# Kernel tuning notes

Measured on AMD Instinct MI355X. Metric: run time of the kernel, lower is better.

The kernel has to match this reference:

```python
import jax, jax.numpy as jnp
import numpy as np

MX_D, MN_D, CENTERS, WIDTH, SLOPE = 10.0, 0.0, 16, 1.0, 0.01
T_STEPS = 3


def _lrelu(x):
    return jax.nn.leaky_relu(x, SLOPE)


def _gauss(d):
    # d: [B,E,1] distances -> [B,E,CENTERS] gaussian radial basis
    mu = jnp.linspace(MN_D, MX_D, CENTERS, dtype=d.dtype)
    return jnp.exp(-jnp.square((d - mu[None, None, :]) / WIDTH))


def _equiv_message(v, idx2, n_recv, W1, W2, b, aw, ab):
    # v: [B,E,F] = concat(sender feats, receiver feats, bond feats).
    # Outer-product expand over receiver-cell axis (einsum with one-hot),
    # permutation-equivariant linear (local term + cell-sum term), LeakyReLU,
    # gather receiver cell, sigmoid attention gate, scatter_add to receivers.
    B, E, _ = v.shape
    O = W1.shape[1]
    oh = jax.nn.one_hot(idx2, n_recv, dtype=v.dtype)                 # [E,N]
    y_loc = jnp.einsum('bef,fo->beo', v, W1)                          # per-cell term
    y_sum = jnp.einsum('bef,fo->beo', v, W2) + b                      # cell-sum term (sum_n v*oh = v)
    y = _lrelu(y_loc[..., None] * oh[None, :, None, :] + y_sum[..., None])  # [B,E,O,N]
    gidx = jnp.broadcast_to(idx2[None, :, None, None], (B, E, O, 1))
    lat = jnp.take_along_axis(y, gidx, axis=3)[..., 0]                # [B,E,O]
    lat = jax.nn.sigmoid(lat @ aw + ab[None, None, :]) * lat          # attention gating
    return jnp.zeros((B, n_recv, O), v.dtype).at[:, idx2].add(lat)    # scatter_add over receivers


def _forward(sites, bonds, sites_p, bonds_sp, bonds_ps,
             se_W, se_b, sep_W, sep_b, ee_W, ee_b, eep_W, eep_b,
             eq_W1_ss, eq_W2_ss, eq_b_ss, att_w_ss, att_b_ss,
             eq_W1_ps, eq_W2_ps, eq_b_ps, att_w_ps, att_b_ps,
             eq_W1_sp, eq_W2_sp, eq_b_sp, att_w_sp, att_b_sp,
             nu_W1, nu_b1, nu_W2, nu_b2, nup_W1, nup_b1, nup_W2, nup_b2,
             p1_W, p1_b, p2a_W, p2a_b, p2b_W, p2b_b, p3_W, p3_b,
             idx1, idx2, idx1_sp, idx2_sp, idx1_ps, idx2_ps):
    s = _lrelu(sites @ se_W + se_b)          # [B,N,D] site embedding
    sp = _lrelu(sites_p @ sep_W + sep_b)     # [B,Np,D] pore embedding
    be = _lrelu(_gauss(bonds) @ ee_W + ee_b)
    bsp = _lrelu(_gauss(bonds_sp) @ eep_W + eep_b)
    bps = _lrelu(_gauss(bonds_ps) @ eep_W + eep_b)
    N, Np = s.shape[1], sp.shape[1]
    for t in range(T_STEPS):  # fixed number of message-passing layers
        v_ss = jnp.concatenate([s[:, idx1], s[:, idx2], be], -1)
        m = _equiv_message(v_ss, idx2, N, eq_W1_ss[t], eq_W2_ss[t], eq_b_ss[t], att_w_ss[t], att_b_ss[t])
        v_ps = jnp.concatenate([sp[:, idx1_ps], s[:, idx2_ps], bps], -1)
        m_ps = _equiv_message(v_ps, idx2_ps, N, eq_W1_ps[t], eq_W2_ps[t], eq_b_ps[t], att_w_ps[t], att_b_ps[t])
        v_sp = jnp.concatenate([s[:, idx1_sp], sp[:, idx2_sp], bsp], -1)
        m_sp = _equiv_message(v_sp, idx2_sp, Np, eq_W1_sp[t], eq_W2_sp[t], eq_b_sp[t], att_w_sp[t], att_b_sp[t])
        h = jnp.concatenate([s, m, m_ps], -1)
        h = _lrelu(_lrelu(h @ nu_W1[t] + nu_b1[t]) @ nu_W2[t] + nu_b2[t])
        s = s + h                              # residual node update (sites)
        hp = jnp.concatenate([sp, m_sp], -1)
        hp = _lrelu(_lrelu(hp @ nup_W1[t] + nup_b1[t]) @ nup_W2[t] + nup_b2[t])
        sp = sp + hp                           # residual node update (pores)
    x = _lrelu(s @ p1_W + p1_b).sum(1)        # sum pool over sites
    x = _lrelu(x @ p2a_W + p2a_b)
    x = _lrelu(x @ p2b_W + p2b_b)
    return x @ p3_W + p3_b                    # [B, out_size]


def setup_inputs():
    key = jax.random.key(0)
    ks = iter(jax.random.split(key, 80))
    B, N, Np, E, Esp = 4, 128, 16, 1280, 1024
    D, C, O, M, T = 32, CENTERS, 32, 64, T_STEPS
    Fin = 2 * D + 16  # sender + receiver + edge embedding

    def nrm(shape, fan):
        return jax.random.normal(next(ks), shape, jnp.float32) / np.float32(np.sqrt(fan))

    inp = {}
    inp['sites'] = jax.random.uniform(next(ks), (B, N, 1), jnp.float32)
    inp['bonds'] = jax.random.uniform(next(ks), (B, E, 1), jnp.float32) * MX_D
    inp['sites_p'] = jax.random.uniform(next(ks), (B, Np, 2), jnp.float32)
    inp['bonds_sp'] = jax.random.uniform(next(ks), (B, Esp, 1), jnp.float32) * MX_D
    inp['bonds_ps'] = jax.random.uniform(next(ks), (B, Esp, 1), jnp.float32) * MX_D
    inp['idx1'] = jax.random.randint(next(ks), (E,), 0, N, jnp.int32)
    inp['idx2'] = jax.random.randint(next(ks), (E,), 0, N, jnp.int32)
    inp['idx1_sp'] = jax.random.randint(next(ks), (Esp,), 0, N, jnp.int32)
    inp['idx2_sp'] = jax.random.randint(next(ks), (Esp,), 0, Np, jnp.int32)
    inp['idx1_ps'] = jax.random.randint(next(ks), (Esp,), 0, Np, jnp.int32)
    inp['idx2_ps'] = jax.random.randint(next(ks), (Esp,), 0, N, jnp.int32)
    # embeddings
    inp['se_W'] = nrm((1, D), 1); inp['se_b'] = nrm((D,), D)
    inp['sep_W'] = nrm((2, D), 2); inp['sep_b'] = nrm((D,), D)
    inp['ee_W'] = nrm((C, 16), C); inp['ee_b'] = nrm((16,), 16)
    inp['eep_W'] = nrm((C, 16), C); inp['eep_b'] = nrm((16,), 16)
    # equivariant message layers (stacked over T steps)
    for suf in ('ss', 'ps', 'sp'):
        inp['eq_W1_' + suf] = nrm((T, Fin, O), Fin)
        inp['eq_W2_' + suf] = nrm((T, Fin, O), Fin)
        inp['eq_b_' + suf] = nrm((T, O), O)
        inp['att_w_' + suf] = nrm((T, O, 1), O)
        inp['att_b_' + suf] = nrm((T, 1), 1)
    # node updates: sites take 2 message streams, pores take 1
    inp['nu_W1'] = nrm((T, D + 2 * O, D), D + 2 * O); inp['nu_b1'] = nrm((T, D), D)
    inp['nu_W2'] = nrm((T, D, D), D); inp['nu_b2'] = nrm((T, D), D)
    inp['nup_W1'] = nrm((T, D + O, D), D + O); inp['nup_b1'] = nrm((T, D), D)
    inp['nup_W2'] = nrm((T, D, D), D); inp['nup_b2'] = nrm((T, D), D)
    # prediction head
    inp['p1_W'] = nrm((D, M), D); inp['p1_b'] = nrm((M,), M)
    inp['p2a_W'] = nrm((M, M), M); inp['p2a_b'] = nrm((M,), M)
    inp['p2b_W'] = nrm((M, M), M); inp['p2b_b'] = nrm((M,), M)
    inp['p3_W'] = nrm((M, 1), M); inp['p3_b'] = nrm((1,), 1)
    return inp


def reference(sites, bonds, sites_p, bonds_sp, bonds_ps,
              se_W, se_b, sep_W, sep_b, ee_W, ee_b, eep_W, eep_b,
              eq_W1_ss, eq_W2_ss, eq_b_ss, att_w_ss, att_b_ss,
              eq_W1_ps, eq_W2_ps, eq_b_ps, att_w_ps, att_b_ps,
              eq_W1_sp, eq_W2_sp, eq_b_sp, att_w_sp, att_b_sp,
              nu_W1, nu_b1, nu_W2, nu_b2, nup_W1, nup_b1, nup_W2, nup_b2,
              p1_W, p1_b, p2a_W, p2a_b, p2b_W, p2b_b, p3_W, p3_b,
              idx1, idx2, idx1_sp, idx2_sp, idx1_ps, idx2_ps):
    return _forward(sites, bonds, sites_p, bonds_sp, bonds_ps,
                    se_W, se_b, sep_W, sep_b, ee_W, ee_b, eep_W, eep_b,
                    eq_W1_ss, eq_W2_ss, eq_b_ss, att_w_ss, att_b_ss,
                    eq_W1_ps, eq_W2_ps, eq_b_ps, att_w_ps, att_b_ps,
                    eq_W1_sp, eq_W2_sp, eq_b_sp, att_w_sp, att_b_sp,
                    nu_W1, nu_b1, nu_W2, nu_b2, nup_W1, nup_b1, nup_W2, nup_b2,
                    p1_W, p1_b, p2a_W, p2a_b, p2b_W, p2b_b, p3_W, p3_b,
                    idx1, idx2, idx1_sp, idx2_sp, idx1_ps, idx2_ps)
```

## Files before the change

### kernel.cpp

```cpp
#include <hip/hip_runtime.h>
#include <math.h>

#define BB   4
#define NN   128
#define NPP  16
#define EEE  1280
#define ESP  1024
#define DD   32
#define CC   16
#define OO   32
#define FIN  80
#define MMM  64
#define TT   3
#define TPB  256

#define MAXDEG_SS 48
#define MAXDEG_SP 192

constexpr int OFF_S    = 0;
constexpr int OFF_SP   = OFF_S   + BB*NN*DD;
constexpr int OFF_BE   = OFF_SP  + BB*NPP*DD;
constexpr int OFF_BSP  = OFF_BE  + BB*EEE*CC;
constexpr int OFF_BPS  = OFF_BSP + BB*ESP*CC;
constexpr int OFF_PRJ  = OFF_BPS + BB*ESP*CC;
constexpr int P_SASS = 0;
constexpr int P_SBSS = P_SASS + BB*NN*OO;
constexpr int P_SBPS = P_SBSS + BB*NN*OO;
constexpr int P_SASP = P_SBPS + BB*NN*OO;
constexpr int P_PAPS = P_SASP + BB*NN*OO;
constexpr int P_PBSP = P_PAPS + BB*NPP*OO;
constexpr int PRJ_SZ = P_PBSP + BB*NPP*OO;
constexpr int OFF_POOL = OFF_PRJ + 2*PRJ_SZ;
constexpr int OFF_CSR  = OFF_POOL + BB*MMM;
constexpr int SS_CNT  = 0;
constexpr int SS_LIST = SS_CNT + NN;
constexpr int PS_CNT  = SS_LIST + NN*MAXDEG_SS;
constexpr int PS_LIST = PS_CNT + NN;
constexpr int SP_CNT  = PS_LIST + NN*MAXDEG_SS;
constexpr int SP_LIST = SP_CNT + NPP;
constexpr int CSR_INTS = SP_LIST + NPP*MAXDEG_SP;
constexpr int TICKET   = CSR_INTS;

__device__ __forceinline__ float lrelu(float x) { return x > 0.f ? x : 0.01f * x; }

__device__ __forceinline__ float dot16(const float* ef, const float* sWe, int o) {
    float4 f0 = *(const float4*)(ef);
    float4 f1 = *(const float4*)(ef + 4);
    float4 f2 = *(const float4*)(ef + 8);
    float4 f3 = *(const float4*)(ef + 12);
    return f0.x*sWe[ 0*32+o] + f0.y*sWe[ 1*32+o] + f0.z*sWe[ 2*32+o] + f0.w*sWe[ 3*32+o]
         + f1.x*sWe[ 4*32+o] + f1.y*sWe[ 5*32+o] + f1.z*sWe[ 6*32+o] + f1.w*sWe[ 7*32+o]
         + f2.x*sWe[ 8*32+o] + f2.y*sWe[ 9*32+o] + f2.z*sWe[10*32+o] + f2.w*sWe[11*32+o]
         + f3.x*sWe[12*32+o] + f3.y*sWe[13*32+o] + f3.z*sWe[14*32+o] + f3.w*sWe[15*32+o];
}

__device__ __forceinline__ float red32(float r) {
#pragma unroll
    for (int mm = 16; mm > 0; mm >>= 1) r += __shfl_xor(r, mm, 32);
    return r;
}

__device__ __forceinline__ void edge_embed(float d, const float* W, const float* bvec, float* out) {
    float g[CC];
#pragma unroll
    for (int c = 0; c < CC; ++c) {
        float mu = (10.0f / 15.0f) * (float)c;
        float z = d - mu;
        g[c] = expf(-z * z);
    }
#pragma unroll
    for (int j = 0; j < CC; ++j) {
        float a = bvec[j];
#pragma unroll
        for (int c = 0; c < CC; ++c) a += g[c] * W[c * CC + j];
        out[j] = lrelu(a);
    }
}

__device__ __forceinline__ void csr_wave(const int* recv, int E, int r,
                                         int* cnt, int* list, int maxdeg, int lane) {
    int base = 0;
    for (int c = 0; c < E; c += 64) {
        const int e = c + lane;
        const bool m = (recv[e] == r);
        const unsigned long long mask = __ballot(m);
        if (m) {
            const int pos = base + __popcll(mask & ((1ull << lane) - 1ull));
            if (pos < maxdeg) list[pos] = e;
        }
        base += (int)__popcll(mask);
    }
    if (lane == 0) cnt[r] = base < maxdeg ? base : maxdeg;
}

__global__ __launch_bounds__(TPB) void k_init(
    const float* sites, const float* bonds, const float* sites_p,
    const float* bonds_sp, const float* bonds_ps,
    const int* idx2, const int* idx2_ps, const int* idx2_sp,
    const float* se_W, const float* se_b, const float* sep_W, const float* sep_b,
    const float* ee_W, const float* ee_b, const float* eep_W, const float* eep_b,
    const float* eqW1_ss, const float* eqW2_ss,
    const float* eqW1_ps, const float* eqW2_ps,
    const float* eqW1_sp, const float* eqW2_sp,
    float* ws)
{
    __shared__ float smem[4416];
    const int blk = blockIdx.x;
    const int tid = threadIdx.x;
    int* csr = (int*)(ws + OFF_CSR);

    if (blk == 0 && tid == 0) csr[TICKET] = 0;

    if (blk < 253) {
        const int totalA = BB*MMM + BB*EEE + BB*ESP + BB*ESP;
        for (int i = blk*TPB + tid; i < totalA; i += 253*TPB) {
            int r = i;
            if (r < BB*MMM) { ws[OFF_POOL + r] = 0.f; continue; }
            r -= BB*MMM;
            if (r < BB*EEE) { edge_embed(bonds[r],    ee_W,  ee_b,  ws + OFF_BE  + r*CC); continue; }
            r -= BB*EEE;
            if (r < BB*ESP) { edge_embed(bonds_sp[r], eep_W, eep_b, ws + OFF_BSP + r*CC); continue; }
            r -= BB*ESP;
            edge_embed(bonds_ps[r], eep_W, eep_b, ws + OFF_BPS + r*CC);
        }
    }
    if (blk < 72) {
        float* prj0 = ws + OFF_PRJ;
        const int el = tid >> 5, o = tid & 31;
        float* sP   = smem;
        float* sRow = smem + 4160;
        if (blk < 64) {
            const int g = blk*8 + el;
            float x = sites[g];
            float v0 = lrelu(x * se_W[o] + se_b[o]);
            ws[OFF_S + g*DD + o] = v0;
            sRow[el*32 + o] = v0;
            for (int i2 = tid; i2 < 4096; i2 += TPB) {
                int m = i2 >> 10, j = i2 & 1023, d = j >> 5, oo = j & 31;
                int row = (m == 1 || m == 2) ? (DD + d) : d;
                float wv;
                if (m < 2)      wv = eqW1_ss[row*OO + oo] + eqW2_ss[row*OO + oo];
                else if (m==2)  wv = eqW1_ps[row*OO + oo] + eqW2_ps[row*OO + oo];
                else            wv = eqW1_sp[row*OO + oo] + eqW2_sp[row*OO + oo];
                sP[i2] = wv;
            }
            __syncthreads();
            float p0=0.f,p1=0.f,p2=0.f,p3=0.f;
#pragma unroll
            for (int d = 0; d < 32; ++d) {
                float sv = sRow[el*32 + d];
                p0 += sv * sP[        d*32 + o];
                p1 += sv * sP[1024 +  d*32 + o];
                p2 += sv * sP[2048 +  d*32 + o];
                p3 += sv * sP[3072 +  d*32 + o];
            }
            prj0[P_SASS + g*OO + o] = p0;
            prj0[P_SBSS + g*OO + o] = p1;
            prj0[P_SBPS + g*OO + o] = p2;
            prj0[P_SASP + g*OO + o] = p3;
        } else {
            const int g = (blk-64)*8 + el;
            float x0 = sites_p[g*2], x1 = sites_p[g*2+1];
            float v0 = lrelu(x0 * sep_W[o] + x1 * sep_W[DD + o] + sep_b[o]);
            ws[OFF_SP + g*DD + o] = v0;
            sRow[el*32 + o] = v0;
            for (int i2 = tid; i2 < 2048; i2 += TPB) {
                int m = i2 >> 10, j = i2 & 1023, d = j >> 5, oo = j & 31;
                int row = (m == 0) ? d : (DD + d);
                float wv;
                if (m == 0) wv = eqW1_ps[row*OO + oo] + eqW2_ps[row*OO + oo];
                else        wv = eqW1_sp[row*OO + oo] + eqW2_sp[row*OO + oo];
                sP[i2] = wv;
            }
            __syncthreads();
            float p0=0.f,p1=0.f;
#pragma unroll
            for (int d = 0; d < 32; ++d) {
                float sv = sRow[el*32 + d];
                p0 += sv * sP[        d*32 + o];
                p1 += sv * sP[1024 +  d*32 + o];
            }
            prj0[P_PAPS + g*OO + o] = p0;
            prj0[P_PBSP + g*OO + o] = p1;
        }
    }
    if (blk >= 72 && blk < 140) {
        const int widx = (blk - 72) * 4 + (tid >> 6);
        const int lane = tid & 63;
        if (widx < NN) {
            csr_wave(idx2, EEE, widx, csr + SS_CNT, csr + SS_LIST + widx*MAXDEG_SS, MAXDEG_SS, lane);
        } else if (widx < 2*NN) {
            const int r = widx - NN;
            csr_wave(idx2_ps, ESP, r, csr + PS_CNT, csr + PS_LIST + r*MAXDEG_SS, MAXDEG_SS, lane);
        } else if (widx < 2*NN + NPP) {
            const int r = widx - 2*NN;
            csr_wave(idx2_sp, ESP, r, csr + SP_CNT, csr + SP_LIST + r*MAXDEG_SP, MAXDEG_SP, lane);
        }
    }
}

__global__ __launch_bounds__(TPB) void k_step(
    const float* eqW1_ss, const float* eqW2_ss, const float* eqb_ss, const float* aw_ss, const float* ab_ss,
    const float* eqW1_ps, const float* eqW2_ps, const float* eqb_ps, const float* aw_ps, const float* ab_ps,
    const float* eqW1_sp, const float* eqW2_sp, const float* eqb_sp, const float* aw_sp, const float* ab_sp,
    const int* idx1, const int* idx1_ps, const int* idx1_sp,
    const float* nuW1, const float* nub1, const float* nuW2, const float* nub2,
    const float* nupW1, const float* nupb1, const float* nupW2, const float* nupb2,
    const float* p1W, const float* p1b,
    const float* p2aW, const float* p2ab, const float* p2bW, const float* p2bb,
    const float* p3W, const float* p3b,
    float* ws, float* out, int t)
{
    __shared__ float sWe1[512], sWe2[512], sRed[512], sH[192], sU[64], sSnew[64];
    __shared__ int sWin;
    const int tid = threadIdx.x, blk = blockIdx.x;
    const int slot = tid >> 5, o = tid & 31;
    const int par = t & 1;
    const float* PRJ  = ws + OFF_PRJ + par * PRJ_SZ;
    float*       PRJn = ws + OFF_PRJ + (par ^ 1) * PRJ_SZ;
    const int* csr = (const int*)(ws + OFF_CSR);

    if (blk < 256) {
        const int r = slot >> 2, q = slot & 3;
        for (int i = tid; i < 512; i += TPB) {
            sWe1[i] = eqW1_ss[t*FIN*OO + 2*DD*OO + i] + eqW2_ss[t*FIN*OO + 2*DD*OO + i];
            sWe2[i] = eqW1_ps[t*FIN*OO + 2*DD*OO + i] + eqW2_ps[t*FIN*OO + 2*DD*OO + i];
        }
        __syncthreads();
        const int g = blk*2 + r, b = g >> 7, n = g & 127;
        const float bias_ss = eqb_ss[t*OO+o], awo_ss = aw_ss[t*OO+o], abs_ss = ab_ss[t];
        const float bias_ps = eqb_ps[t*OO+o], awo_ps = aw_ps[t*OO+o], abs_ps = ab_ps[t];
        const float sb_ss = PRJ[P_SBSS + g*OO + o];
        const float sb_ps = PRJ[P_SBPS + g*OO + o];
        const float* SAss = PRJ + P_SASS + b*(NN*OO);
        const float* PAps = PRJ + P_PAPS + b*(NPP*OO);
        const float* BEb  = ws + OFF_BE  + b*(EEE*CC);
        const float* BPSb = ws + OFF_BPS + b*(ESP*CC);
        float acc_ss = 0.f, acc_ps = 0.f;
        {
            const int cnt = csr[SS_CNT + n];
            const int* lst = csr + SS_LIST + n*MAXDEG_SS;
            for (int k = q; k < cnt; k += 4) {
                const int e = lst[k];
                const int s1 = idx1[e];
                float a = bias_ss + sb_ss + SAss[s1*OO + o] + dot16(BEb + e*CC, sWe1, o);
                float u = lrelu(a);
                float rr = red32(u * awo_ss);
                acc_ss += u / (1.f + expf(-(rr + abs_ss)));
            }
        }
        {
            const int cnt = csr[PS_CNT + n];
            const int* lst = csr + PS_LIST + n*MAXDEG_SS;
            for (int k = q; k < cnt; k += 4) {
                const int e = lst[k];
                const int s1 = idx1_ps[e];
                float a = bias_ps + sb_ps + PAps[s1*OO + o] + dot16(BPSb + e*CC, sWe2, o);
                float u = lrelu(a);
                float rr = red32(u * awo_ps);
                acc_ps += u / (1.f + expf(-(rr + abs_ps)));
            }
        }
        sRed[slot*64 + o]      = acc_ss;
        sRed[slot*64 + 32 + o] = acc_ps;
        if (tid < 64) sH[(tid>>5)*96 + (tid&31)] = ws[OFF_S + (blk*2 + (tid>>5))*DD + (tid&31)];
        __syncthreads();
        if (tid < 128) {
            const int r2 = tid >> 6, c = tid & 63;
            sH[r2*96 + 32 + c] = sRed[(r2*4  )*64 + c] + sRed[(r2*4+1)*64 + c]
                               + sRed[(r2*4+2)*64 + c] + sRed[(r2*4+3)*64 + c];
        }
        __syncthreads();
        if (tid < 64) {
            const int r2 = tid >> 5, oo = tid & 31;
            const float* W1 = nuW1 + t*(96*32);
            float a = nub1[t*32 + oo];
#pragma unroll
            for (int f = 0; f < 96; ++f) a += sH[r2*96 + f] * W1[f*32 + oo];
            sU[r2*32 + oo] = lrelu(a);
        }
        __syncthreads();
        if (tid < 64) {
            const int r2 = tid >> 5, oo = tid & 31;
            const float* W2 = nuW2 + t*(32*32);
            float a = nub2[t*32 + oo];
#pragma unroll
            for (int k2 = 0; k2 < 32; ++k2) a += sU[r2*32 + k2] * W2[k2*32 + oo];
            const float snew = sH[r2*96 + oo] + lrelu(a);
            ws[OFF_S + (blk*2 + r2)*DD + oo] = snew;
            sSnew[r2*32 + oo] = snew;
        }
        __syncthreads();
        if (t < TT-1) {
            const int tn = t + 1;
            const int r2 = slot >> 2, m = slot & 3;
            const int g2 = blk*2 + r2;
            const float *w1m, *w2m; float* dst;
            if (m == 0)      { w1m = eqW1_ss + tn*FIN*OO;         w2m = eqW2_ss + tn*FIN*OO;         dst = PRJn + P_SASS; }
            else if (m == 1) { w1m = eqW1_ss + tn*FIN*OO + DD*OO; w2m = eqW2_ss + tn*FIN*OO + DD*OO; dst = PRJn + P_SBSS; }
            else if (m == 2) { w1m = eqW1_ps + tn*FIN*OO + DD*OO; w2m = eqW2_ps + tn*FIN*OO + DD*OO; dst = PRJn + P_SBPS; }
            else             { w1m = eqW1_sp + tn*FIN*OO;         w2m = eqW2_sp + tn*FIN*OO;         dst = PRJn + P_SASP; }
            float a = 0.f;
#pragma unroll
            for (int d = 0; d < 32; ++d) a += sSnew[r2*32 + d] * (w1m[d*OO + o] + w2m[d*OO + o]);
            dst[g2*OO + o] = a;
        } else {
            if (tid < 128) {
                const int r2 = tid >> 6, mm = tid & 63;
                const int g2 = blk*2 + r2, b2 = g2 >> 7;
                float a = p1b[mm];
#pragma unroll
                for (int d = 0; d < 32; ++d) a += sSnew[r2*32 + d] * p1W[d*MMM + mm];
                atomicAdd(&ws[OFF_POOL + b2*MMM + mm], lrelu(a));
            }
            __syncthreads();
            if (tid == 0) {
                int* ticket = (int*)(ws + OFF_CSR) + TICKET;
                int p = __hip_atomic_fetch_add(ticket, 1, __ATOMIC_ACQ_REL, __HIP_MEMORY_SCOPE_AGENT);
                sWin = (p == 255) ? 1 : 0;
            }
            __syncthreads();
            if (sWin) {
                float* sx = sWe1;
                float* sy = sWe2;
                float* sz = sRed;
                sx[tid] = __hip_atomic_load(&ws[OFF_POOL + tid], __ATOMIC_RELAXED, __HIP_MEMORY_SCOPE_AGENT);
                __syncthreads();
                const int b2 = tid >> 6, mm = tid & 63;
                float a = p2ab[mm];
#pragma unroll
                for (int k = 0; k < MMM; ++k) a += sx[b2*64 + k] * p2aW[k*MMM + mm];
                sy[tid] = lrelu(a);
                __syncthreads();
                a = p2bb[mm];
#pragma unroll
                for (int k = 0; k < MMM; ++k) a += sy[b2*64 + k] * p2bW[k*MMM + mm];
                sz[tid] = lrelu(a);
                __syncthreads();
                if (tid < BB) {
                    float acc = p3b[0];
#pragma unroll
                    for (int k = 0; k < MMM; ++k) acc += sz[tid*64 + k] * p3W[k];
                    out[tid] = acc;
                }
            }
        }
    } else {
        for (int i = tid; i < 512; i += TPB)
            sWe1[i] = eqW1_sp[t*FIN*OO + 2*DD*OO + i] + eqW2_sp[t*FIN*OO + 2*DD*OO + i];
        __syncthreads();
        const int g = blk - 256, b = g >> 4, p = g & 15;
        const float bias_sp = eqb_sp[t*OO+o], awo_sp = aw_sp[t*OO+o], abs_sp = ab_sp[t];
        const float sb_sp = PRJ[P_PBSP + g*OO + o];
        const float* SAsp = PRJ + P_SASP + b*(NN*OO);
        const float* BSPb = ws + OFF_BSP + b*(ESP*CC);
        float acc_sp = 0.f;
        {
            const int cnt = csr[SP_CNT + p];
            const int* lst = csr + SP_LIST + p*MAXDEG_SP;
            for (int k = slot; k < cnt; k += 8) {
                const int e = lst[k];
                const int s1 = idx1_sp[e];
                float a = bias_sp + sb_sp + SAsp[s1*OO + o] + dot16(BSPb + e*CC, sWe1, o);
                float u = lrelu(a);
                float rr = red32(u * awo_sp);
                acc_sp += u / (1.f + expf(-(rr + abs_sp)));
            }
        }
        sRed[slot*32 + o] = acc_sp;
        if (tid < 32) sH[tid] = ws[OFF_SP + g*DD + tid];
        __syncthreads();
        if (tid < 32) {
            float mv = 0.f;
#pragma unroll
            for (int s2 = 0; s2 < 8; ++s2) mv += sRed[s2*32 + tid];
            sH[32 + tid] = mv;
        }
        __syncthreads();
        if (tid < 32) {
            const float* W1 = nupW1 + t*(64*32);
            float a = nupb1[t*32 + tid];
#pragma unroll
            for (int f = 0; f < 64; ++f) a += sH[f] * W1[f*32 + tid];
            sU[tid] = lrelu(a);
        }
        __syncthreads();
        if (tid < 32) {
            const float* W2 = nupW2 + t*(32*32);
            float a = nupb2[t*32 + tid];
#pragma unroll
            for (int k2 = 0; k2 < 32; ++k2) a += sU[k2] * W2[k2*32 + tid];
            const float snew = sH[tid] + lrelu(a);
            ws[OFF_SP + g*DD + tid] = snew;
            sSnew[tid] = snew;
        }
        __syncthreads();
        if (t < TT-1 && tid < 64) {
            const int tn = t + 1;
            const int m = tid >> 5, oo = tid & 31;
            const float *w1m, *w2m; float* dst;
            if (m == 0) { w1m = eqW1_ps + tn*FIN*OO;         w2m = eqW2_ps + tn*FIN*OO;         dst = PRJn + P_PAPS; }
            else        { w1m = eqW1_sp + tn*FIN*OO + DD*OO; w2m = eqW2_sp + tn*FIN*OO + DD*OO; dst = PRJn + P_PBSP; }
            float a = 0.f;
#pragma unroll
            for (int d = 0; d < 32; ++d) a += sSnew[d] * (w1m[d*OO + oo] + w2m[d*OO + oo]);
            dst[g*OO + oo] = a;
        }
    }
}

extern "C" void kernel_launch(void* const* d_in, const int* in_sizes, int n_in,
                              void* d_out, int out_size, void* d_ws, size_t ws_size,
                              hipStream_t stream) {
    (void)in_sizes; (void)n_in; (void)out_size; (void)ws_size;
    const float* sites    = (const float*)d_in[0];
    const float* bonds    = (const float*)d_in[1];
    const float* sites_p  = (const float*)d_in[2];
    const float* bonds_sp = (const float*)d_in[3];
    const float* bonds_ps = (const float*)d_in[4];
    const int* idx1    = (const int*)d_in[5];
    const int* idx2    = (const int*)d_in[6];
    const int* idx1_sp = (const int*)d_in[7];
    const int* idx2_sp = (const int*)d_in[8];
    const int* idx1_ps = (const int*)d_in[9];
    const int* idx2_ps = (const int*)d_in[10];
    const float* se_W  = (const float*)d_in[11];
    const float* se_b  = (const float*)d_in[12];
    const float* sep_W = (const float*)d_in[13];
    const float* sep_b = (const float*)d_in[14];
    const float* ee_W  = (const float*)d_in[15];
    const float* ee_b  = (const float*)d_in[16];
    const float* eep_W = (const float*)d_in[17];
    const float* eep_b = (const float*)d_in[18];
    const float* eqW1_ss = (const float*)d_in[19];
    const float* eqW2_ss = (const float*)d_in[20];
    const float* eqb_ss  = (const float*)d_in[21];
    const float* aw_ss   = (const float*)d_in[22];
    const float* ab_ss   = (const float*)d_in[23];
    const float* eqW1_ps = (const float*)d_in[24];
    const float* eqW2_ps = (const float*)d_in[25];
    const float* eqb_ps  = (const float*)d_in[26];
    const float* aw_ps   = (const float*)d_in[27];
    const float* ab_ps   = (const float*)d_in[28];
    const float* eqW1_sp = (const float*)d_in[29];
    const float* eqW2_sp = (const float*)d_in[30];
    const float* eqb_sp  = (const float*)d_in[31];
    const float* aw_sp   = (const float*)d_in[32];
    const float* ab_sp   = (const float*)d_in[33];
    const float* nuW1  = (const float*)d_in[34];
    const float* nub1  = (const float*)d_in[35];
    const float* nuW2  = (const float*)d_in[36];
    const float* nub2  = (const float*)d_in[37];
    const float* nupW1 = (const float*)d_in[38];
    const float* nupb1 = (const float*)d_in[39];
    const float* nupW2 = (const float*)d_in[40];
    const float* nupb2 = (const float*)d_in[41];
    const float* p1W  = (const float*)d_in[42];
    const float* p1b  = (const float*)d_in[43];
    const float* p2aW = (const float*)d_in[44];
    const float* p2ab = (const float*)d_in[45];
    const float* p2bW = (const float*)d_in[46];
    const float* p2bb = (const float*)d_in[47];
    const float* p3W  = (const float*)d_in[48];
    const float* p3b  = (const float*)d_in[49];

    float* ws  = (float*)d_ws;
    float* out = (float*)d_out;

    k_init<<<256, TPB, 0, stream>>>(sites, bonds, sites_p, bonds_sp, bonds_ps,
                                    idx2, idx2_ps, idx2_sp,
                                    se_W, se_b, sep_W, sep_b, ee_W, ee_b, eep_W, eep_b,
                                    eqW1_ss, eqW2_ss, eqW1_ps, eqW2_ps, eqW1_sp, eqW2_sp, ws);
    for (int t = 0; t < TT; ++t) {
        k_step<<<320, TPB, 0, stream>>>(
            eqW1_ss, eqW2_ss, eqb_ss, aw_ss, ab_ss,
            eqW1_ps, eqW2_ps, eqb_ps, aw_ps, ab_ps,
            eqW1_sp, eqW2_sp, eqb_sp, aw_sp, ab_sp,
            idx1, idx1_ps, idx1_sp,
            nuW1, nub1, nuW2, nub2, nupW1, nupb1, nupW2, nupb2,
            p1W, p1b, p2aW, p2ab, p2bW, p2bb, p3W, p3b,
            ws, out, t);
    }
}
```

Baseline: 55.53 us.

## Restructure step kernel to one node per 512-thread block with packed edge-sender pairs

Each step block now handles one site node with 512 threads, splitting site-site and pore-site edges across separate warp groups, where before one block covered two nodes. Pore blocks use 16 slots. The CSR build now stores (edge, sender) int2 pairs, which removes the dependent idx1 gather inside the edge loop. The per-edge 16-wide weight vector is kept in registers instead of shared memory, which removes the shared-memory staging and its barrier. The grid grows to 576 blocks, giving more parallelism but more per-block overhead and higher register pressure from the larger blocks.

```diff
diff --git a/kernel.cpp b/kernel.cpp
--- a/kernel.cpp
+++ b/kernel.cpp
@@ -13,6 +13,7 @@
 #define MMM  64
 #define TT   3
 #define TPB  256
+#define SPB  512
 
 #define MAXDEG_SS 48
 #define MAXDEG_SP 192
@@ -33,25 +34,24 @@
 constexpr int OFF_POOL = OFF_PRJ + 2*PRJ_SZ;
 constexpr int OFF_CSR  = OFF_POOL + BB*MMM;
 constexpr int SS_CNT  = 0;
-constexpr int SS_LIST = SS_CNT + NN;
-constexpr int PS_CNT  = SS_LIST + NN*MAXDEG_SS;
-constexpr int PS_LIST = PS_CNT + NN;
-constexpr int SP_CNT  = PS_LIST + NN*MAXDEG_SS;
-constexpr int SP_LIST = SP_CNT + NPP;
-constexpr int CSR_INTS = SP_LIST + NPP*MAXDEG_SP;
-constexpr int TICKET   = CSR_INTS;
+constexpr int PS_CNT  = SS_CNT + NN;
+constexpr int SP_CNT  = PS_CNT + NN;
+constexpr int TICKET  = SP_CNT + NPP;
+constexpr int SS_PAIR = 274;
+constexpr int PS_PAIR = SS_PAIR + NN*MAXDEG_SS*2;
+constexpr int SP_PAIR = PS_PAIR + NN*MAXDEG_SS*2;
 
 __device__ __forceinline__ float lrelu(float x) { return x > 0.f ? x : 0.01f * x; }
 
-__device__ __forceinline__ float dot16(const float* ef, const float* sWe, int o) {
+__device__ __forceinline__ float dot16r(const float* ef, const float* we) {
     float4 f0 = *(const float4*)(ef);
     float4 f1 = *(const float4*)(ef + 4);
     float4 f2 = *(const float4*)(ef + 8);
     float4 f3 = *(const float4*)(ef + 12);
-    return f0.x*sWe[ 0*32+o] + f0.y*sWe[ 1*32+o] + f0.z*sWe[ 2*32+o] + f0.w*sWe[ 3*32+o]
-         + f1.x*sWe[ 4*32+o] + f1.y*sWe[ 5*32+o] + f1.z*sWe[ 6*32+o] + f1.w*sWe[ 7*32+o]
-         + f2.x*sWe[ 8*32+o] + f2.y*sWe[ 9*32+o] + f2.z*sWe[10*32+o] + f2.w*sWe[11*32+o]
-         + f3.x*sWe[12*32+o] + f3.y*sWe[13*32+o] + f3.z*sWe[14*32+o] + f3.w*sWe[15*32+o];
+    return f0.x*we[ 0] + f0.y*we[ 1] + f0.z*we[ 2] + f0.w*we[ 3]
+         + f1.x*we[ 4] + f1.y*we[ 5] + f1.z*we[ 6] + f1.w*we[ 7]
+         + f2.x*we[ 8] + f2.y*we[ 9] + f2.z*we[10] + f2.w*we[11]
+         + f3.x*we[12] + f3.y*we[13] + f3.z*we[14] + f3.w*we[15];
 }
 
 __device__ __forceinline__ float red32(float r) {
@@ -77,8 +77,8 @@
     }
 }
 
-__device__ __forceinline__ void csr_wave(const int* recv, int E, int r,
-                                         int* cnt, int* list, int maxdeg, int lane) {
+__device__ __forceinline__ void csr_wave(const int* recv, const int* send, int E, int r,
+                                         int* cnt, int2* pair, int maxdeg, int lane) {
     int base = 0;
     for (int c = 0; c < E; c += 64) {
         const int e = c + lane;
@@ -86,7 +86,7 @@
         const unsigned long long mask = __ballot(m);
         if (m) {
             const int pos = base + __popcll(mask & ((1ull << lane) - 1ull));
-            if (pos < maxdeg) list[pos] = e;
+            if (pos < maxdeg) pair[pos] = make_int2(e, send[e]);
         }
         base += (int)__popcll(mask);
     }
@@ -96,7 +96,8 @@
 __global__ __launch_bounds__(TPB) void k_init(
     const float* sites, const float* bonds, const float* sites_p,
     const float* bonds_sp, const float* bonds_ps,
-    const int* idx2, const int* idx2_ps, const int* idx2_sp,
+    const int* idx1, const int* idx2, const int* idx1_ps, const int* idx2_ps,
+    const int* idx1_sp, const int* idx2_sp,
     const float* se_W, const float* se_b, const float* sep_W, const float* sep_b,
     const float* ee_W, const float* ee_b, const float* eep_W, const float* eep_b,
     const float* eqW1_ss, const float* eqW2_ss,
@@ -188,22 +189,24 @@
         const int widx = (blk - 72) * 4 + (tid >> 6);
         const int lane = tid & 63;
         if (widx < NN) {
-            csr_wave(idx2, EEE, widx, csr + SS_CNT, csr + SS_LIST + widx*MAXDEG_SS, MAXDEG_SS, lane);
+            csr_wave(idx2, idx1, EEE, widx, csr + SS_CNT,
+                     (int2*)(csr + SS_PAIR) + widx*MAXDEG_SS, MAXDEG_SS, lane);
         } else if (widx < 2*NN) {
             const int r = widx - NN;
-            csr_wave(idx2_ps, ESP, r, csr + PS_CNT, csr + PS_LIST + r*MAXDEG_SS, MAXDEG_SS, lane);
+            csr_wave(idx2_ps, idx1_ps, ESP, r, csr + PS_CNT,
+                     (int2*)(csr + PS_PAIR) + r*MAXDEG_SS, MAXDEG_SS, lane);
         } else if (widx < 2*NN + NPP) {
             const int r = widx - 2*NN;
-            csr_wave(idx2_sp, ESP, r, csr + SP_CNT, csr + SP_LIST + r*MAXDEG_SP, MAXDEG_SP, lane);
-        }
-    }
-}
-
-__global__ __launch_bounds__(TPB) void k_step(
+            csr_wave(idx2_sp, idx1_sp, ESP, r, csr + SP_CNT,
+                     (int2*)(csr + SP_PAIR) + r*MAXDEG_SP, MAXDEG_SP, lane);
+        }
+    }
+}
+
+__global__ __launch_bounds__(SPB) void k_step(
     const float* eqW1_ss, const float* eqW2_ss, const float* eqb_ss, const float* aw_ss, const float* ab_ss,
     const float* eqW1_ps, const float* eqW2_ps, const float* eqb_ps, const float* aw_ps, const float* ab_ps,
     const float* eqW1_sp, const float* eqW2_sp, const float* eqb_sp, const float* aw_sp, const float* ab_sp,
-    const int* idx1, const int* idx1_ps, const int* idx1_sp,
     const float* nuW1, const float* nub1, const float* nuW2, const float* nub2,
     const float* nupW1, const float* nupb1, const float* nupW2, const float* nupb2,
     const float* p1W, const float* p1b,
@@ -211,7 +214,9 @@
     const float* p3W, const float* p3b,
     float* ws, float* out, int t)
 {
-    __shared__ float sWe1[512], sWe2[512], sRed[512], sH[192], sU[64], sSnew[64];
+    __shared__ float sRed[768];
+    __shared__ float sH[96], sU[32], sSnew[32];
+    __shared__ float sHy[256], sHz[256];
     __shared__ int sWin;
     const int tid = threadIdx.x, blk = blockIdx.x;
     const int slot = tid >> 5, o = tid & 31;
@@ -220,160 +225,152 @@
     float*       PRJn = ws + OFF_PRJ + (par ^ 1) * PRJ_SZ;
     const int* csr = (const int*)(ws + OFF_CSR);
 
-    if (blk < 256) {
-        const int r = slot >> 2, q = slot & 3;
-        for (int i = tid; i < 512; i += TPB) {
-            sWe1[i] = eqW1_ss[t*FIN*OO + 2*DD*OO + i] + eqW2_ss[t*FIN*OO + 2*DD*OO + i];
-            sWe2[i] = eqW1_ps[t*FIN*OO + 2*DD*OO + i] + eqW2_ps[t*FIN*OO + 2*DD*OO + i];
-        }
-        __syncthreads();
-        const int g = blk*2 + r, b = g >> 7, n = g & 127;
-        const float bias_ss = eqb_ss[t*OO+o], awo_ss = aw_ss[t*OO+o], abs_ss = ab_ss[t];
-        const float bias_ps = eqb_ps[t*OO+o], awo_ps = aw_ps[t*OO+o], abs_ps = ab_ps[t];
-        const float sb_ss = PRJ[P_SBSS + g*OO + o];
-        const float sb_ps = PRJ[P_SBPS + g*OO + o];
-        const float* SAss = PRJ + P_SASS + b*(NN*OO);
-        const float* PAps = PRJ + P_PAPS + b*(NPP*OO);
-        const float* BEb  = ws + OFF_BE  + b*(EEE*CC);
-        const float* BPSb = ws + OFF_BPS + b*(ESP*CC);
-        float acc_ss = 0.f, acc_ps = 0.f;
-        {
-            const int cnt = csr[SS_CNT + n];
-            const int* lst = csr + SS_LIST + n*MAXDEG_SS;
-            for (int k = q; k < cnt; k += 4) {
-                const int e = lst[k];
-                const int s1 = idx1[e];
-                float a = bias_ss + sb_ss + SAss[s1*OO + o] + dot16(BEb + e*CC, sWe1, o);
-                float u = lrelu(a);
-                float rr = red32(u * awo_ss);
-                acc_ss += u / (1.f + expf(-(rr + abs_ss)));
-            }
-        }
-        {
-            const int cnt = csr[PS_CNT + n];
-            const int* lst = csr + PS_LIST + n*MAXDEG_SS;
-            for (int k = q; k < cnt; k += 4) {
-                const int e = lst[k];
-                const int s1 = idx1_ps[e];
-                float a = bias_ps + sb_ps + PAps[s1*OO + o] + dot16(BPSb + e*CC, sWe2, o);
-                float u = lrelu(a);
-                float rr = red32(u * awo_ps);
-                acc_ps += u / (1.f + expf(-(rr + abs_ps)));
-            }
-        }
-        sRed[slot*64 + o]      = acc_ss;
-        sRed[slot*64 + 32 + o] = acc_ps;
-        if (tid < 64) sH[(tid>>5)*96 + (tid&31)] = ws[OFF_S + (blk*2 + (tid>>5))*DD + (tid&31)];
-        __syncthreads();
-        if (tid < 128) {
-            const int r2 = tid >> 6, c = tid & 63;
-            sH[r2*96 + 32 + c] = sRed[(r2*4  )*64 + c] + sRed[(r2*4+1)*64 + c]
-                               + sRed[(r2*4+2)*64 + c] + sRed[(r2*4+3)*64 + c];
-        }
+    if (blk < 512) {
+        const int g = blk, b = g >> 7, n = g & 127;
+        const bool is_ss = slot < 8;
+        const int q = slot & 7;
+        const float* w1p = is_ss ? eqW1_ss : eqW1_ps;
+        const float* w2p = is_ss ? eqW2_ss : eqW2_ps;
+        const float* wa = w1p + t*FIN*OO + 2*DD*OO + o;
+        const float* wb = w2p + t*FIN*OO + 2*DD*OO + o;
+        float we[16];
+#pragma unroll
+        for (int c = 0; c < 16; ++c) we[c] = wa[c*OO] + wb[c*OO];
+        const float bias = (is_ss ? eqb_ss : eqb_ps)[t*OO + o];
+        const float awo  = (is_ss ? aw_ss  : aw_ps )[t*OO + o];
+        const float abv  = (is_ss ? ab_ss  : ab_ps )[t];
+        const float sb   = PRJ[(is_ss ? P_SBSS : P_SBPS) + g*OO + o];
+        const float* SAb = is_ss ? (PRJ + P_SASS + b*(NN*OO))
+                                 : (PRJ + P_PAPS + b*(NPP*OO));
+        const float* EFb = is_ss ? (ws + OFF_BE  + b*(EEE*CC))
+                                 : (ws + OFF_BPS + b*(ESP*CC));
+        const int cnt = is_ss ? csr[SS_CNT + n] : csr[PS_CNT + n];
+        const int2* lst = is_ss ? ((const int2*)(csr + SS_PAIR) + n*MAXDEG_SS)
+                                : ((const int2*)(csr + PS_PAIR) + n*MAXDEG_SS);
+        float acc = 0.f;
+        for (int k = q; k < cnt; k += 8) {
+            const int2 es = lst[k];
+            float a = bias + sb + SAb[es.y*OO + o] + dot16r(EFb + es.x*CC, we);
+            float u = lrelu(a);
+            float rr = red32(u * awo);
+            acc += u / (1.f + expf(-(rr + abv)));
+        }
+        sRed[slot*32 + o] = acc;
+        if (tid < 32) sH[tid] = ws[OFF_S + g*DD + tid];
         __syncthreads();
         if (tid < 64) {
             const int r2 = tid >> 5, oo = tid & 31;
+            float mv = 0.f;
+#pragma unroll
+            for (int j = 0; j < 8; ++j) mv += sRed[(r2*8 + j)*32 + oo];
+            sH[32 + r2*32 + oo] = mv;
+        }
+        __syncthreads();
+        if (tid < 32) {
             const float* W1 = nuW1 + t*(96*32);
-            float a = nub1[t*32 + oo];
-#pragma unroll
-            for (int f = 0; f < 96; ++f) a += sH[r2*96 + f] * W1[f*32 + oo];
-            sU[r2*32 + oo] = lrelu(a);
-        }
-        __syncthreads();
-        if (tid < 64) {
-            const int r2 = tid >> 5, oo = tid & 31;
+            float a = nub1[t*32 + tid];
+#pragma unroll
+            for (int f = 0; f < 96; ++f) a += sH[f] * W1[f*32 + tid];
+            sU[tid] = lrelu(a);
+        }
+        __syncthreads();
+        if (tid < 32) {
             const float* W2 = nuW2 + t*(32*32);
-            float a = nub2[t*32 + oo];
-#pragma unroll
-            for (int k2 = 0; k2 < 32; ++k2) a += sU[r2*32 + k2] * W2[k2*32 + oo];
-            const float snew = sH[r2*96 + oo] + lrelu(a);
-            ws[OFF_S + (blk*2 + r2)*DD + oo] = snew;
-            sSnew[r2*32 + oo] = snew;
+            float a = nub2[t*32 + tid];
+#pragma unroll
+            for (int k2 = 0; k2 < 32; ++k2) a += sU[k2] * W2[k2*32 + tid];
+            const float snew = sH[tid] + lrelu(a);
+            ws[OFF_S + g*DD + tid] = snew;
+            sSnew[tid] = snew;
         }
         __syncthreads();
         if (t < TT-1) {
-            const int tn = t + 1;
-            const int r2 = slot >> 2, m = slot & 3;
-            const int g2 = blk*2 + r2;
-            const float *w1m, *w2m; float* dst;
-            if (m == 0)      { w1m = eqW1_ss + tn*FIN*OO;         w2m = eqW2_ss + tn*FIN*OO;         dst = PRJn + P_SASS; }
-            else if (m == 1) { w1m = eqW1_ss + tn*FIN*OO + DD*OO; w2m = eqW2_ss + tn*FIN*OO + DD*OO; dst = PRJn + P_SBSS; }
-            else if (m == 2) { w1m = eqW1_ps + tn*FIN*OO + DD*OO; w2m = eqW2_ps + tn*FIN*OO + DD*OO; dst = PRJn + P_SBPS; }
-            else             { w1m = eqW1_sp + tn*FIN*OO;         w2m = eqW2_sp + tn*FIN*OO;         dst = PRJn + P_SASP; }
-            float a = 0.f;
-#pragma unroll
-            for (int d = 0; d < 32; ++d) a += sSnew[r2*32 + d] * (w1m[d*OO + o] + w2m[d*OO + o]);
-            dst[g2*OO + o] = a;
+            if (tid < 128) {
+                const int tn = t + 1;
+                const int m = slot;
+                const float *w1m, *w2m; float* dst;
+                if (m == 0)      { w1m = eqW1_ss + tn*FIN*OO;         w2m = eqW2_ss + tn*FIN*OO;         dst = PRJn + P_SASS; }
+                else if (m == 1) { w1m = eqW1_ss + tn*FIN*OO + DD*OO; w2m = eqW2_ss + tn*FIN*OO + DD*OO; dst = PRJn + P_SBSS; }
+                else if (m == 2) { w1m = eqW1_ps + tn*FIN*OO + DD*OO; w2m = eqW2_ps + tn*FIN*OO + DD*OO; dst = PRJn + P_SBPS; }
+                else             { w1m = eqW1_sp + tn*FIN*OO;         w2m = eqW2_sp + tn*FIN*OO;         dst = PRJn + P_SASP; }
+                float a = 0.f;
+#pragma unroll
+                for (int d = 0; d < 32; ++d) a += sSnew[d] * (w1m[d*OO + o] + w2m[d*OO + o]);
+                dst[g*OO + o] = a;
+            }
         } else {
-            if (tid < 128) {
-                const int r2 = tid >> 6, mm = tid & 63;
-                const int g2 = blk*2 + r2, b2 = g2 >> 7;
-                float a = p1b[mm];
-#pragma unroll
-                for (int d = 0; d < 32; ++d) a += sSnew[r2*32 + d] * p1W[d*MMM + mm];
-                atomicAdd(&ws[OFF_POOL + b2*MMM + mm], lrelu(a));
+            if (tid < 64) {
+                float a = p1b[tid];
+#pragma unroll
+                for (int d = 0; d < 32; ++d) a += sSnew[d] * p1W[d*MMM + tid];
+                atomicAdd(&ws[OFF_POOL + b*MMM + tid], lrelu(a));
             }
             __syncthreads();
             if (tid == 0) {
                 int* ticket = (int*)(ws + OFF_CSR) + TICKET;
                 int p = __hip_atomic_fetch_add(ticket, 1, __ATOMIC_ACQ_REL, __HIP_MEMORY_SCOPE_AGENT);
-                sWin = (p == 255) ? 1 : 0;
+                sWin = (p == 511) ? 1 : 0;
             }
             __syncthreads();
             if (sWin) {
-                float* sx = sWe1;
-                float* sy = sWe2;
-                float* sz = sRed;
-                sx[tid] = __hip_atomic_load(&ws[OFF_POOL + tid], __ATOMIC_RELAXED, __HIP_MEMORY_SCOPE_AGENT);
+                float* sx = sRed;
+                if (tid < 256)
+                    sx[tid] = __hip_atomic_load(&ws[OFF_POOL + tid], __ATOMIC_RELAXED, __HIP_MEMORY_SCOPE_AGENT);
                 __syncthreads();
-                const int b2 = tid >> 6, mm = tid & 63;
-                float a = p2ab[mm];
-#pragma unroll
-                for (int k = 0; k < MMM; ++k) a += sx[b2*64 + k] * p2aW[k*MMM + mm];
-                sy[tid] = lrelu(a);
+                if (tid < 256) {
+                    const int b2 = tid >> 6, mm = tid & 63;
+                    float a = p2ab[mm];
+#pragma unroll
+                    for (int k = 0; k < MMM; ++k) a += sx[b2*64 + k] * p2aW[k*MMM + mm];
+                    sHy[tid] = lrelu(a);
+                }
                 __syncthreads();
-                a = p2bb[mm];
-#pragma unroll
-                for (int k = 0; k < MMM; ++k) a += sy[b2*64 + k] * p2bW[k*MMM + mm];
-                sz[tid] = lrelu(a);
+                if (tid < 256) {
+                    const int b2 = tid >> 6, mm = tid & 63;
+                    float a = p2bb[mm];
+#pragma unroll
+                    for (int k = 0; k < MMM; ++k) a += sHy[b2*64 + k] * p2bW[k*MMM + mm];
+                    sHz[tid] = lrelu(a);
+                }
                 __syncthreads();
                 if (tid < BB) {
-                    float acc = p3b[0];
-#pragma unroll
-                    for (int k = 0; k < MMM; ++k) acc += sz[tid*64 + k] * p3W[k];
-                    out[tid] = acc;
+                    float acc2 = p3b[0];
+#pragma unroll
+                    for (int k = 0; k < MMM; ++k) acc2 += sHz[tid*64 + k] * p3W[k];
+                    out[tid] = acc2;
                 }
             }
         }
     } else {
-        for (int i = tid; i < 512; i += TPB)
-            sWe1[i] = eqW1_sp[t*FIN*OO + 2*DD*OO + i] + eqW2_sp[t*FIN*OO + 2*DD*OO + i];
-        __syncthreads();
-        const int g = blk - 256, b = g >> 4, p = g & 15;
-        const float bias_sp = eqb_sp[t*OO+o], awo_sp = aw_sp[t*OO+o], abs_sp = ab_sp[t];
-        const float sb_sp = PRJ[P_PBSP + g*OO + o];
-        const float* SAsp = PRJ + P_SASP + b*(NN*OO);
-        const float* BSPb = ws + OFF_BSP + b*(ESP*CC);
-        float acc_sp = 0.f;
-        {
-            const int cnt = csr[SP_CNT + p];
-            const int* lst = csr + SP_LIST + p*MAXDEG_SP;
-            for (int k = slot; k < cnt; k += 8) {
-                const int e = lst[k];
-                const int s1 = idx1_sp[e];
-                float a = bias_sp + sb_sp + SAsp[s1*OO + o] + dot16(BSPb + e*CC, sWe1, o);
-                float u = lrelu(a);
-                float rr = red32(u * awo_sp);
-                acc_sp += u / (1.f + expf(-(rr + abs_sp)));
-            }
-        }
-        sRed[slot*32 + o] = acc_sp;
+        const int g = blk - 512, b = g >> 4, p = g & 15;
+        const float* wa = eqW1_sp + t*FIN*OO + 2*DD*OO + o;
+        const float* wb = eqW2_sp + t*FIN*OO + 2*DD*OO + o;
+        float we[16];
+#pragma unroll
+        for (int c = 0; c < 16; ++c) we[c] = wa[c*OO] + wb[c*OO];
+        const float bias = eqb_sp[t*OO + o];
+        const float awo  = aw_sp[t*OO + o];
+        const float abv  = ab_sp[t];
+        const float sb   = PRJ[P_PBSP + g*OO + o];
+        const float* SAb = PRJ + P_SASP + b*(NN*OO);
+        const float* EFb = ws + OFF_BSP + b*(ESP*CC);
+        const int cnt = csr[SP_CNT + p];
+        const int2* lst = (const int2*)(csr + SP_PAIR) + p*MAXDEG_SP;
+        float acc = 0.f;
+        for (int k = slot; k < cnt; k += 16) {
+            const int2 es = lst[k];
+            float a = bias + sb + SAb[es.y*OO + o] + dot16r(EFb + es.x*CC, we);
+            float u = lrelu(a);
+            float rr = red32(u * awo);
+            acc += u / (1.f + expf(-(rr + abv)));
+        }
+        sRed[slot*32 + o] = acc;
         if (tid < 32) sH[tid] = ws[OFF_SP + g*DD + tid];
         __syncthreads();
         if (tid < 32) {
             float mv = 0.f;
 #pragma unroll
-            for (int s2 = 0; s2 < 8; ++s2) mv += sRed[s2*32 + tid];
+            for (int j = 0; j < 16; ++j) mv += sRed[j*32 + tid];
             sH[32 + tid] = mv;
         }
         __syncthreads();
@@ -397,14 +394,14 @@
         __syncthreads();
         if (t < TT-1 && tid < 64) {
             const int tn = t + 1;
-            const int m = tid >> 5, oo = tid & 31;
+            const int m = slot;
             const float *w1m, *w2m; float* dst;
             if (m == 0) { w1m = eqW1_ps + tn*FIN*OO;         w2m = eqW2_ps + tn*FIN*OO;         dst = PRJn + P_PAPS; }
             else        { w1m = eqW1_sp + tn*FIN*OO + DD*OO; w2m = eqW2_sp + tn*FIN*OO + DD*OO; dst = PRJn + P_PBSP; }
             float a = 0.f;
 #pragma unroll
-            for (int d = 0; d < 32; ++d) a += sSnew[d] * (w1m[d*OO + oo] + w2m[d*OO + oo]);
-            dst[g*OO + oo] = a;
+            for (int d = 0; d < 32; ++d) a += sSnew[d] * (w1m[d*OO + o] + w2m[d*OO + o]);
+            dst[g*OO + o] = a;
         }
     }
 }
@@ -468,15 +465,14 @@
     float* out = (float*)d_out;
 
     k_init<<<256, TPB, 0, stream>>>(sites, bonds, sites_p, bonds_sp, bonds_ps,
-                                    idx2, idx2_ps, idx2_sp,
+                                    idx1, idx2, idx1_ps, idx2_ps, idx1_sp, idx2_sp,
                                     se_W, se_b, sep_W, sep_b, ee_W, ee_b, eep_W, eep_b,
                                     eqW1_ss, eqW2_ss, eqW1_ps, eqW2_ps, eqW1_sp, eqW2_sp, ws);
     for (int t = 0; t < TT; ++t) {
-        k_step<<<320, TPB, 0, stream>>>(
+        k_step<<<576, SPB, 0, stream>>>(
             eqW1_ss, eqW2_ss, eqb_ss, aw_ss, ab_ss,
             eqW1_ps, eqW2_ps, eqb_ps, aw_ps, ab_ps,
             eqW1_sp, eqW2_sp, eqb_sp, aw_sp, ab_sp,
-            idx1, idx1_ps, idx1_sp,
             nuW1, nub1, nuW2, nub2, nupW1, nupb1, nupW2, nupb2,
             p1W, p1b, p2aW, p2ab, p2bW, p2bb, p3W, p3b,
             ws, out, t);
```

Result: slower. 58.92 us (+6.1%).
